# Kernel optimization log

Hardware: AMD Instinct MI355X
Metric: run time of the kernel (lower is better)

## Reference

```python
import jax, jax.numpy as jnp
import numpy as np

# Module hyperparameters (from init_kwargs)
N_HEAD = 16
D_K = 64
D_V = 64
TEMPERATURE = 0.7
TOP_K = 32
NEG_MIN = jnp.finfo(jnp.float32).min


def setup_inputs() -> dict:
    key = jax.random.key(0)
    ks = jax.random.split(key, 7)
    B, L, E = 2, 2048, 1024
    return {
        "q": jax.random.normal(ks[0], (B, L, E), jnp.float32),
        "k": jax.random.normal(ks[1], (B, L, E), jnp.float32),
        "v": jax.random.normal(ks[2], (B, L, D_V), jnp.float32),
        "w_q": jax.random.normal(ks[3], (N_HEAD * D_K, E), jnp.float32) * (E ** -0.5),
        "w_k": jax.random.normal(ks[4], (N_HEAD * D_K, E), jnp.float32) * (E ** -0.5),
        "w_v": jax.random.normal(ks[5], (N_HEAD * D_V, D_V), jnp.float32) * (D_V ** -0.5),
        "w_fc": jax.random.normal(ks[6], (D_V, N_HEAD * D_V), jnp.float32) * ((N_HEAD * D_V) ** -0.5),
    }


def _topk_restrict(logits):
    # Keep exactly TOP_K entries per row (scatter of top-k indices), fill rest with dtype min.
    B, H, Lq, Lk = logits.shape
    _, idx = jax.lax.top_k(logits, TOP_K)  # [B,H,Lq,TOP_K]
    bb = jnp.arange(B)[:, None, None, None]
    hh = jnp.arange(H)[None, :, None, None]
    qq = jnp.arange(Lq)[None, None, :, None]
    keep = jnp.zeros(logits.shape, bool).at[bb, hh, qq, idx].set(True)
    return jnp.where(keep, logits, NEG_MIN)


def reference(q, k, v, w_q, w_k, w_v, w_fc):
    B, Lq, _ = q.shape
    Lk = k.shape[1]
    Lv = v.shape[1]
    # Projections (bias-free linears), split heads: [B, H, L, d]
    q_proj = (q @ w_q.T).reshape(B, Lq, N_HEAD, D_K).transpose(0, 2, 1, 3)
    k_proj = (k @ w_k.T).reshape(B, Lk, N_HEAD, D_K).transpose(0, 2, 1, 3)
    v_proj = (v @ w_v.T).reshape(B, Lv, N_HEAD, D_V).transpose(0, 2, 1, 3)
    # Scaled QK^T in float32, then temperature scaling.
    logits = jnp.einsum("bhqd,bhkd->bhqk", q_proj / (D_K ** 0.5), k_proj).astype(jnp.float32)
    logits = logits / TEMPERATURE
    # Top-k restriction of attention logits (query_mask_flat=None -> applied to all queries).
    logits = _topk_restrict(logits)
    # Softmax selection; dropout is identity in eval / p=0.
    attn_probs = jax.nn.softmax(logits, axis=-1).astype(v.dtype)
    mixed = jnp.einsum("bhqk,bhkd->bhqd", attn_probs, v_proj)
    out = mixed.transpose(0, 2, 1, 3).reshape(B, Lq, N_HEAD * D_V)
    output = out @ w_fc.T
    return output, attn_probs
```

## Files before the change

### kernel.cpp

```cpp
#include <hip/hip_runtime.h>
#include <stdint.h>
#include <float.h>

constexpr int L = 2048;
constexpr int H = 16;
constexpr float SCALE = 0.17857142857142858f;
constexpr int OUT0 = 2 * 2048 * 64;
constexpr float QSTEP = 0.0625f;

typedef float f32x4 __attribute__((ext_vector_type(4)));
typedef short s16x8 __attribute__((ext_vector_type(8)));
typedef unsigned short u16x8 __attribute__((ext_vector_type(8)));
typedef _Float16 h16x8 __attribute__((ext_vector_type(8)));

__device__ __forceinline__ unsigned f2sort(float f) {
  unsigned u = __float_as_uint(f);
  return (u & 0x80000000u) ? ~u : (u | 0x80000000u);
}
__device__ __forceinline__ void lds_fence() {
  __asm__ __volatile__("s_waitcnt lgkmcnt(0)" ::: "memory");
}

__device__ __forceinline__ int wave_isum_dpp(int x) {
#define DPP_ADDI(CTRL) x += __builtin_amdgcn_update_dpp(0, x, CTRL, 0xf, 0xf, true);
  DPP_ADDI(0x111) DPP_ADDI(0x112) DPP_ADDI(0x114)
  DPP_ADDI(0x118) DPP_ADDI(0x142) DPP_ADDI(0x143)
#undef DPP_ADDI
  return __builtin_amdgcn_readlane(x, 63);
}
__device__ __forceinline__ float wave_fsum_dpp(float x) {
  int xi = __builtin_bit_cast(int, x);
#define DPP_ADDF(CTRL)                                                      \
  {                                                                         \
    int _s = __builtin_amdgcn_update_dpp(0, xi, CTRL, 0xf, 0xf, true);      \
    x = x + __builtin_bit_cast(float, _s);                                  \
    xi = __builtin_bit_cast(int, x);                                        \
  }
  DPP_ADDF(0x111) DPP_ADDF(0x112) DPP_ADDF(0x114)
  DPP_ADDF(0x118) DPP_ADDF(0x142) DPP_ADDF(0x143)
#undef DPP_ADDF
  return __builtin_bit_cast(float, __builtin_amdgcn_readlane(xi, 63));
}
__device__ __forceinline__ float wave_fmax_dpp(float x) {
  int xi = __builtin_bit_cast(int, x);
#define DPP_MAXF(CTRL)                                                      \
  {                                                                         \
    int _s = __builtin_amdgcn_update_dpp(xi, xi, CTRL, 0xf, 0xf, false);    \
    x = fmaxf(x, __builtin_bit_cast(float, _s));                            \
    xi = __builtin_bit_cast(int, x);                                        \
  }
  DPP_MAXF(0x111) DPP_MAXF(0x112) DPP_MAXF(0x114)
  DPP_MAXF(0x118) DPP_MAXF(0x142) DPP_MAXF(0x143)
#undef DPP_MAXF
  return __builtin_bit_cast(float, __builtin_amdgcn_readlane(xi, 63));
}
__device__ __forceinline__ int wave_imin_dpp(int x) {
#define DPP_MINI(CTRL)                                                      \
  {                                                                         \
    int _s = __builtin_amdgcn_update_dpp(x, x, CTRL, 0xf, 0xf, false);      \
    x = min(x, _s);                                                         \
  }
  DPP_MINI(0x111) DPP_MINI(0x112) DPP_MINI(0x114)
  DPP_MINI(0x118) DPP_MINI(0x142) DPP_MINI(0x143)
#undef DPP_MINI
  return __builtin_amdgcn_readlane(x, 63);
}

__device__ __forceinline__ void gload_lds16(const void* g, void* l) {
  __builtin_amdgcn_global_load_lds((const __attribute__((address_space(1))) void*)g,
                                   (__attribute__((address_space(3))) void*)l, 16, 0, 0);
}

__global__ __launch_bounds__(256) void split_kernel(
    const float* __restrict__ q, const float* __restrict__ k,
    const float* __restrict__ wq, const float* __restrict__ wk,
    unsigned short* __restrict__ qh, unsigned short* __restrict__ ql,
    unsigned short* __restrict__ kh, unsigned short* __restrict__ kl,
    unsigned short* __restrict__ wqh, unsigned short* __restrict__ wql,
    unsigned short* __restrict__ wkh, unsigned short* __restrict__ wkl) {
  const int y = blockIdx.y;
  const float* src = (y == 0) ? q : (y == 1) ? k : (y == 2) ? wq : wk;
  unsigned short* dh = (y == 0) ? qh : (y == 1) ? kh : (y == 2) ? wqh : wkh;
  unsigned short* dl = (y == 0) ? ql : (y == 1) ? kl : (y == 2) ? wql : wkl;
  const int n = (y < 2) ? (4096 * 1024) : (1024 * 1024);
  int idx = (blockIdx.x * 256 + threadIdx.x) * 4;
  const int stride = gridDim.x * 256 * 4;
  for (; idx < n; idx += stride) {
    float4 v = *(const float4*)(src + idx);
    float xs[4] = {v.x, v.y, v.z, v.w};
    unsigned short hs[4], ls[4];
#pragma unroll
    for (int i = 0; i < 4; ++i) {
      float x = xs[i] * 256.0f;
      _Float16 hh = (_Float16)x;
      float r = x - (float)hh;
      _Float16 ll = (_Float16)r;
      hs[i] = __builtin_bit_cast(unsigned short, hh);
      ls[i] = __builtin_bit_cast(unsigned short, ll);
    }
    *(ushort4*)(dh + idx) = make_ushort4(hs[0], hs[1], hs[2], hs[3]);
    *(ushort4*)(dl + idx) = make_ushort4(ls[0], ls[1], ls[2], ls[3]);
  }
}

__global__ __launch_bounds__(256, 2) void proj_split_kernel(
    const unsigned short* __restrict__ QH, const unsigned short* __restrict__ QL,
    const unsigned short* __restrict__ KH, const unsigned short* __restrict__ KL,
    const unsigned short* __restrict__ WQH, const unsigned short* __restrict__ WQL,
    const unsigned short* __restrict__ WKH, const unsigned short* __restrict__ WKL,
    float* __restrict__ QP, float* __restrict__ KP,
    unsigned short* __restrict__ Q16, unsigned short* __restrict__ K16) {
  __shared__ unsigned short sh[4][128 * 64];
  const int t = threadIdx.x;
  const int z = blockIdx.z;
  const int m0 = blockIdx.y * 128;
  const int n0 = blockIdx.x * 128;
  const unsigned short* xh = z ? KH : QH;
  const unsigned short* xl = z ? KL : QL;
  const unsigned short* wh = z ? WKH : WQH;
  const unsigned short* wl = z ? WKL : WQL;
  float* Y = z ? KP : QP;
  unsigned short* Y16 = z ? K16 : Q16;
  const unsigned short* mats[4] = {xh + (size_t)m0 * 1024, xl + (size_t)m0 * 1024,
                                   wh + (size_t)n0 * 1024, wl + (size_t)n0 * 1024};
  const int wv = t >> 6, lane = t & 63;
  const int wm = (wv & 1) * 64, wn = (wv >> 1) * 64;
  const int fr = lane & 15, quad = lane >> 4;
  f32x4 acc[16];
#pragma unroll
  for (int i = 0; i < 16; ++i) acc[i] = (f32x4){0.f, 0.f, 0.f, 0.f};

#define STAGE(cc)                                                              \
  {                                                                            \
    const int k0s = (cc) * 64;                                                 \
    _Pragma("unroll") for (int j = 0; j < 16; ++j) {                           \
      const int mat = j >> 2;                                                  \
      const int idx = (j & 3) * 256 + t;                                       \
      const int r = idx >> 3, p = idx & 7;                                     \
      const int sb = p ^ (r & 7);                                              \
      gload_lds16(mats[mat] + (size_t)r * 1024 + k0s + sb * 8, &sh[mat][idx * 8]); \
    }                                                                          \
  }

  STAGE(0);
  for (int c = 0; c < 16; ++c) {
    __syncthreads();
    h16x8 ah[2][4], alv[2][4], bh[2][4], blv[2][4];
#pragma unroll
    for (int kh2 = 0; kh2 < 2; ++kh2) {
#pragma unroll
      for (int mi = 0; mi < 4; ++mi) {
        int row = wm + mi * 16 + fr;
        int pp = (kh2 * 4 + quad) ^ (row & 7);
        ah[kh2][mi]  = *(const h16x8*)&sh[0][row * 64 + pp * 8];
        alv[kh2][mi] = *(const h16x8*)&sh[1][row * 64 + pp * 8];
      }
#pragma unroll
      for (int ni = 0; ni < 4; ++ni) {
        int row = wn + ni * 16 + fr;
        int pp = (kh2 * 4 + quad) ^ (row & 7);
        bh[kh2][ni]  = *(const h16x8*)&sh[2][row * 64 + pp * 8];
        blv[kh2][ni] = *(const h16x8*)&sh[3][row * 64 + pp * 8];
      }
    }
    __syncthreads();
    if (c < 15) STAGE(c + 1);
#pragma unroll
    for (int kh2 = 0; kh2 < 2; ++kh2)
#pragma unroll
      for (int mi = 0; mi < 4; ++mi)
#pragma unroll
        for (int ni = 0; ni < 4; ++ni) {
          acc[mi * 4 + ni] = __builtin_amdgcn_mfma_f32_16x16x32_f16(ah[kh2][mi], bh[kh2][ni], acc[mi * 4 + ni], 0, 0, 0);
          acc[mi * 4 + ni] = __builtin_amdgcn_mfma_f32_16x16x32_f16(ah[kh2][mi], blv[kh2][ni], acc[mi * 4 + ni], 0, 0, 0);
          acc[mi * 4 + ni] = __builtin_amdgcn_mfma_f32_16x16x32_f16(alv[kh2][mi], bh[kh2][ni], acc[mi * 4 + ni], 0, 0, 0);
        }
  }
#undef STAGE
#pragma unroll
  for (int mi = 0; mi < 4; ++mi)
#pragma unroll
    for (int ni = 0; ni < 4; ++ni) {
      int col = n0 + wn + ni * 16 + fr;
      int h = col >> 6, d = col & 63;
#pragma unroll
      for (int r = 0; r < 4; ++r) {
        int m = m0 + wm + mi * 16 + quad * 4 + r;
        int b = m >> 11, l = m & 2047;
        size_t off = (((size_t)b * H + h) * L + l) * 64 + d;
        float val = acc[mi * 4 + ni][r] * (1.0f / 65536.0f);
        Y[off] = val;
        _Float16 hf = (_Float16)val;
        Y16[off] = __builtin_bit_cast(unsigned short, hf);
      }
    }
}

template <int K, bool EMIT>
__global__ __launch_bounds__(256) void proj_kernel(const float* __restrict__ X,
                                                   const float* __restrict__ W,
                                                   float* __restrict__ Y,
                                                   unsigned short* __restrict__ Yb,
                                                   float bscale) {
  __shared__ float As[16][128];
  __shared__ float Bs[16][64];
  const int t = threadIdx.x;
  const int tx = t & 15;
  const int ty = t >> 4;
  const int m0 = blockIdx.y * 128;
  const int n0 = blockIdx.x * 64;
  const int ar = t >> 1, ac = (t & 1) * 8;
  const int br = t >> 2, bc = (t & 3) * 4;
  const float* xg = X + (size_t)(m0 + ar) * K + ac;
  const float* wg = W + (size_t)(n0 + br) * K + bc;
  float acc[8][4] = {};
  for (int k0 = 0; k0 < K; k0 += 16) {
    float4 a0 = *(const float4*)(xg + k0);
    float4 a1 = *(const float4*)(xg + k0 + 4);
    float4 b0 = *(const float4*)(wg + k0);
    __syncthreads();
    As[ac + 0][ar] = a0.x; As[ac + 1][ar] = a0.y; As[ac + 2][ar] = a0.z; As[ac + 3][ar] = a0.w;
    As[ac + 4][ar] = a1.x; As[ac + 5][ar] = a1.y; As[ac + 6][ar] = a1.z; As[ac + 7][ar] = a1.w;
    Bs[bc + 0][br] = b0.x; Bs[bc + 1][br] = b0.y; Bs[bc + 2][br] = b0.z; Bs[bc + 3][br] = b0.w;
    __syncthreads();
#pragma unroll
    for (int kk = 0; kk < 16; ++kk) {
      float4 av0 = *(const float4*)&As[kk][ty * 8];
      float4 av1 = *(const float4*)&As[kk][ty * 8 + 4];
      float4 bv = *(const float4*)&Bs[kk][tx * 4];
      float ar8[8] = {av0.x, av0.y, av0.z, av0.w, av1.x, av1.y, av1.z, av1.w};
      float br4[4] = {bv.x, bv.y, bv.z, bv.w};
#pragma unroll
      for (int i = 0; i < 8; ++i)
#pragma unroll
        for (int j = 0; j < 4; ++j) acc[i][j] = fmaf(ar8[i], br4[j], acc[i][j]);
    }
  }
  const int n = n0 + tx * 4;
  const int h = n >> 6, d = n & 63;
#pragma unroll
  for (int i = 0; i < 8; ++i) {
    int mm = m0 + ty * 8 + i;
    int b = mm >> 11, l = mm & 2047;
    size_t off = (((size_t)b * H + h) * L + l) * 64 + d;
    *(float4*)&Y[off] = make_float4(acc[i][0], acc[i][1], acc[i][2], acc[i][3]);
  }
}

constexpr int ALD = 72;
constexpr int CTB = 136;

__global__ __launch_bounds__(256) void alogits_kernel(const unsigned short* __restrict__ Qb,
                                                      const unsigned short* __restrict__ Kb,
                                                      char* __restrict__ AL) {
  __shared__ union {
    unsigned short qk[2][128 * ALD];
    char ct[128 * CTB];
  } sh;
  const int t = threadIdx.x;
  const int bh = blockIdx.z;
  const int m0 = blockIdx.y * 128, n0 = blockIdx.x * 128;
  const unsigned short* Qg = Qb + (size_t)bh * L * 64 + (size_t)m0 * 64;
  const unsigned short* Kg = Kb + (size_t)bh * L * 64 + (size_t)n0 * 64;
#pragma unroll
  for (int i = 0; i < 4; ++i) {
    int blk = t * 4 + i;
    int r = blk >> 3, lb = blk & 7;
    *(u16x8*)&sh.qk[0][r * ALD + lb * 8] = *(const u16x8*)&Qg[r * 64 + lb * 8];
    *(u16x8*)&sh.qk[1][r * ALD + lb * 8] = *(const u16x8*)&Kg[r * 64 + lb * 8];
  }
  __syncthreads();
  const int wv = t >> 6, lane = t & 63;
  const int wm = (wv & 1) * 64, wn = (wv >> 1) * 64;
  const int fr = lane & 15, quad = lane >> 4;
  f32x4 acc[16];
#pragma unroll
  for (int i = 0; i < 16; ++i) acc[i] = (f32x4){0.f, 0.f, 0.f, 0.f};
#pragma unroll
  for (int kh = 0; kh < 2; ++kh) {
    h16x8 a[4], b[4];
#pragma unroll
    for (int mi = 0; mi < 4; ++mi)
      a[mi] = *(const h16x8*)&sh.qk[0][(wm + mi * 16 + fr) * ALD + kh * 32 + quad * 8];
#pragma unroll
    for (int ni = 0; ni < 4; ++ni)
      b[ni] = *(const h16x8*)&sh.qk[1][(wn + ni * 16 + fr) * ALD + kh * 32 + quad * 8];
#pragma unroll
    for (int mi = 0; mi < 4; ++mi)
#pragma unroll
      for (int ni = 0; ni < 4; ++ni)
        acc[mi * 4 + ni] = __builtin_amdgcn_mfma_f32_16x16x32_f16(
            a[mi], b[ni], acc[mi * 4 + ni], 0, 0, 0);
  }
  __syncthreads();
#pragma unroll
  for (int mi = 0; mi < 4; ++mi)
#pragma unroll
    for (int ni = 0; ni < 4; ++ni) {
      int col = wn + ni * 16 + fr;
#pragma unroll
      for (int r = 0; r < 4; ++r) {
        int rowl = wm + mi * 16 + quad * 4 + r;
        float sc = acc[mi * 4 + ni][r] * 2.8571428571428572f;
        sc = fminf(fmaxf(sc, -127.0f), 127.0f);
        sh.ct[rowl * CTB + col] = (char)__float2int_rn(sc);
      }
    }
  __syncthreads();
  char* Abase = AL + (size_t)bh * L * L;
  const int rq = lane >> 4;
  const int cq = (lane & 15) * 8;
#pragma unroll
  for (int it = 0; it < 8; ++it) {
    int row = wv * 32 + it * 4 + rq;
    uint2 v8 = *(const uint2*)&sh.ct[row * CTB + cq];
    __builtin_nontemporal_store(v8.x, (unsigned*)&Abase[(size_t)(m0 + row) * L + n0 + cq]);
    __builtin_nontemporal_store(v8.y, (unsigned*)&Abase[(size_t)(m0 + row) * L + n0 + cq + 4]);
  }
}

__global__ __launch_bounds__(256) void select_kernel(const char* __restrict__ AL,
                                                     const float* __restrict__ Qp,
                                                     const float* __restrict__ Kp,
                                                     const float* __restrict__ Vp,
                                                     float* __restrict__ Probs,
                                                     float* __restrict__ Mixed) {
  __shared__ float prow[4][2048];
  __shared__ float qbuf[4][64];
  __shared__ int ibufc[4][64];
  __shared__ float pbuf[4][32];
  __shared__ int ibuf[4][32];
  const int lane = threadIdx.x & 63;
  const int w = threadIdx.x >> 6;
  const int row = blockIdx.x * 4 + w;
  const int bh = row >> 11;
  const int q = row & 2047;
  const unsigned long long below = (lane == 63) ? 0x7fffffffffffffffull
                                                : ((1ull << lane) - 1ull);
  const unsigned* Arow = (const unsigned*)(AL + (size_t)row * 2048);

  int li[32];
#pragma unroll
  for (int u2 = 0; u2 < 8; ++u2) {
    unsigned dw = __builtin_nontemporal_load(Arow + u2 * 64 + lane);
#pragma unroll
    for (int b = 0; b < 4; ++b)
      li[u2 * 4 + b] = (int)((char)(dw >> (8 * b)));
  }
#pragma unroll
  for (int u = 0; u < 32; ++u) prow[w][u * 64 + lane] = 0.f;
  if (lane < 16)
    *(float4*)&qbuf[w][lane * 4] = *(const float4*)&Qp[((size_t)bh * L + q) * 64 + lane * 4];

  int tlo = -128, thi = 128;
#pragma unroll
  for (int it = 0; it < 8; ++it) {
    int mid = (tlo + thi) >> 1;
    int c = 0;
#pragma unroll
    for (int u = 0; u < 32; ++u) c += (li[u] >= mid) ? 1 : 0;
    c = wave_isum_dpp(c);
    if (c >= 32) tlo = mid; else thi = mid;
  }
  const int t32 = tlo;

  int theta = t32;
  int c2 = 0;
  const int margs[5] = {6, 4, 2, 1, 0};
#pragma unroll
  for (int a = 0; a < 5; ++a) {
    int th = t32 - margs[a];
    int c = 0;
#pragma unroll
    for (int u = 0; u < 32; ++u) c += (li[u] >= th) ? 1 : 0;
    c = wave_isum_dpp(c);
    theta = th; c2 = c;
    if (c <= 64) break;
  }
  if (c2 > 64) c2 = 64;

  {
    int base = 0;
#pragma unroll
    for (int u = 0; u < 32; ++u) {
      bool cd = li[u] >= theta;
      unsigned long long mk = __ballot(cd);
      if (cd) {
        int s = base + __popcll(mk & below);
        if (s < 64) ibufc[w][s] = ((u >> 2) * 64 + lane) * 4 + (u & 3);
      }
      base += __popcll(mk);
    }
  }
  lds_fence();

  int myi = (lane < c2) ? ibufc[w][lane] : 0x7fffffff;
  float vex = -FLT_MAX;
  if (lane < c2) {
    const float4* K4 = (const float4*)(Kp + ((size_t)bh * L + myi) * 64);
    const float4* Q4 = (const float4*)&qbuf[w][0];
    float acc = 0.f;
#pragma unroll
    for (int dq = 0; dq < 16; ++dq) {
      float4 kv = K4[dq];
      float4 qv = Q4[dq];
      acc = fmaf(qv.x, kv.x, acc);
      acc = fmaf(qv.y, kv.y, acc);
      acc = fmaf(qv.z, kv.z, acc);
      acc = fmaf(qv.w, kv.w, acc);
    }
    vex = (acc * 0.125f) / 0.7f;
  }

  const unsigned sk = f2sort(vex);
  unsigned tb = 0;
#pragma unroll
  for (int bit = 31; bit >= 0; --bit) {
    unsigned cand = tb | (1u << bit);
    int cnt = (int)__popcll(__ballot(sk >= cand));
    if (cnt >= 32) tb = cand;
  }
  bool kept = sk > tb;
  {
    int cnt_gt = (int)__popcll(__ballot(kept));
    int need = 32 - cnt_gt;
    unsigned long long tiem = __ballot(sk == tb);
    if ((int)__popcll(tiem) <= need) {
      kept = kept || (sk == tb);
    } else {
      bool isT = (sk == tb);
      for (int r = 0; r < need; ++r) {
        int mi = wave_imin_dpp(isT ? myi : 0x7fffffff);
        if (isT && myi == mi) { kept = true; isT = false; }
      }
    }
  }

  float vmax = wave_fmax_dpp(vex);
  float e = kept ? __expf(vex - vmax) : 0.f;
  float S = wave_fsum_dpp(e);
  float p = e / S;
  {
    unsigned long long km = __ballot(kept);
    int slot = (int)__popcll(km & below);
    if (kept) {
      pbuf[w][slot] = p;
      ibuf[w][slot] = myi;
      prow[w][myi] = p;
    }
  }
  lds_fence();

  float* Prow = Probs + (size_t)row * 2048;
#pragma unroll
  for (int u = 0; u < 32; ++u)
    __builtin_nontemporal_store(prow[w][u * 64 + lane], Prow + u * 64 + lane);

  const float* Vb = Vp + (size_t)bh * L * 64;
  float accv = 0.f;
#pragma unroll
  for (int i = 0; i < 32; ++i)
    accv = fmaf(pbuf[w][i], Vb[(size_t)ibuf[w][i] * 64 + lane], accv);
  const int bb = bh >> 4, hh = bh & 15;
  Mixed[((size_t)(bb * 2048 + q)) * 1024 + hh * 64 + lane] = accv;
}

__global__ __launch_bounds__(256) void fc_kernel(const float* __restrict__ Mx,
                                                 const float* __restrict__ Wfc,
                                                 float* __restrict__ Out) {
  __shared__ float As[32][64];
  __shared__ float Ws[64][64];
  const int t = threadIdx.x;
  const int tx = t & 15;
  const int ty = t >> 4;
  const int m0 = blockIdx.x * 32;
  float acc[2][4] = {};
  for (int k0 = 0; k0 < 1024; k0 += 64) {
    __syncthreads();
    {
      int lin = t * 8;
      int rr = lin >> 6, kk = lin & 63;
      *(float4*)&As[rr][kk] = *(const float4*)&Mx[(size_t)(m0 + rr) * 1024 + k0 + kk];
      *(float4*)&As[rr][kk + 4] = *(const float4*)&Mx[(size_t)(m0 + rr) * 1024 + k0 + kk + 4];
    }
    {
      int n = t >> 2;
      int kq = (t & 3) * 16;
#pragma unroll
      for (int u = 0; u < 4; ++u) {
        float4 wv = *(const float4*)&Wfc[(size_t)n * 1024 + k0 + kq + u * 4];
        Ws[kq + u * 4 + 0][n] = wv.x;
        Ws[kq + u * 4 + 1][n] = wv.y;
        Ws[kq + u * 4 + 2][n] = wv.z;
        Ws[kq + u * 4 + 3][n] = wv.w;
      }
    }
    __syncthreads();
#pragma unroll
    for (int kk = 0; kk < 64; ++kk) {
      float a0 = As[ty][kk], a1 = As[ty + 16][kk];
      float4 wv = *(const float4*)&Ws[kk][tx * 4];
      float wr[4] = {wv.x, wv.y, wv.z, wv.w};
#pragma unroll
      for (int j = 0; j < 4; ++j) {
        acc[0][j] = fmaf(a0, wr[j], acc[0][j]);
        acc[1][j] = fmaf(a1, wr[j], acc[1][j]);
      }
    }
  }
#pragma unroll
  for (int i = 0; i < 2; ++i) {
    int mm = m0 + ty + i * 16;
    *(float4*)&Out[(size_t)mm * 64 + tx * 4] =
        make_float4(acc[i][0], acc[i][1], acc[i][2], acc[i][3]);
  }
}

extern "C" void kernel_launch(void* const* d_in, const int* in_sizes, int n_in,
                              void* d_out, int out_size, void* d_ws, size_t ws_size,
                              hipStream_t stream) {
  const float* q    = (const float*)d_in[0];
  const float* k    = (const float*)d_in[1];
  const float* v    = (const float*)d_in[2];
  const float* w_q  = (const float*)d_in[3];
  const float* w_k  = (const float*)d_in[4];
  const float* w_v  = (const float*)d_in[5];
  const float* w_fc = (const float*)d_in[6];

  float* out = (float*)d_out;
  float* probs = out + OUT0;

  float* ws = (float*)d_ws;
  float* q_proj = ws;
  float* k_proj = ws + 4194304;
  float* v_proj = ws + 8388608;
  float* mixed  = ws + 12582912;
  unsigned short* qb = (unsigned short*)(ws + 16777216);
  unsigned short* kb = (unsigned short*)(ws + 18874368);
  char* al = (char*)(ws + 20971520);

  unsigned short* qh  = (unsigned short*)((char*)d_ws + 234881024);
  unsigned short* ql  = qh + 4194304;
  unsigned short* kh  = ql + 4194304;
  unsigned short* kl  = kh + 4194304;
  unsigned short* wqh = kl + 4194304;
  unsigned short* wql = wqh + 1048576;
  unsigned short* wkh = wql + 1048576;
  unsigned short* wkl = wkh + 1048576;

  dim3 blk(256);
  split_kernel<<<dim3(1024, 4), blk, 0, stream>>>(q, k, w_q, w_k,
                                                  qh, ql, kh, kl, wqh, wql, wkh, wkl);
  proj_split_kernel<<<dim3(8, 32, 2), blk, 0, stream>>>(qh, ql, kh, kl,
                                                        wqh, wql, wkh, wkl,
                                                        q_proj, k_proj, qb, kb);
  proj_kernel<64, false><<<dim3(16, 32), blk, 0, stream>>>(v, w_v, v_proj, nullptr, 1.0f);
  alogits_kernel<<<dim3(16, 16, 32), blk, 0, stream>>>(qb, kb, al);
  select_kernel<<<dim3(16384), blk, 0, stream>>>(al, q_proj, k_proj, v_proj, probs, mixed);
  fc_kernel<<<dim3(128), blk, 0, stream>>>(mixed, w_fc, out);
}
```

Measured before the change: 855.2 us.

## Split select kernel into top-k selection and scatter/PV kernels

The select kernel no longer holds a 32KB shared-memory probability row or writes the dense probs and PV product. It now emits 32 (index, prob) pairs per row to a workspace buffer, and a new scatter_pv_kernel builds the dense row, writes probs and computes the V mix. The int8 logit stores and loads also switch from nontemporal to regular accesses, which may let the logits stay in cache between kernels. The split frees LDS so the selection stage can run at higher occupancy, at the cost of an extra launch and a pair round-trip through memory.

```diff
diff --git a/kernel.cpp b/kernel.cpp
--- a/kernel.cpp
+++ b/kernel.cpp
@@ -314,22 +314,17 @@
   for (int it = 0; it < 8; ++it) {
     int row = wv * 32 + it * 4 + rq;
     uint2 v8 = *(const uint2*)&sh.ct[row * CTB + cq];
-    __builtin_nontemporal_store(v8.x, (unsigned*)&Abase[(size_t)(m0 + row) * L + n0 + cq]);
-    __builtin_nontemporal_store(v8.y, (unsigned*)&Abase[(size_t)(m0 + row) * L + n0 + cq + 4]);
+    *(unsigned*)&Abase[(size_t)(m0 + row) * L + n0 + cq] = v8.x;
+    *(unsigned*)&Abase[(size_t)(m0 + row) * L + n0 + cq + 4] = v8.y;
   }
 }
 
 __global__ __launch_bounds__(256) void select_kernel(const char* __restrict__ AL,
                                                      const float* __restrict__ Qp,
                                                      const float* __restrict__ Kp,
-                                                     const float* __restrict__ Vp,
-                                                     float* __restrict__ Probs,
-                                                     float* __restrict__ Mixed) {
-  __shared__ float prow[4][2048];
+                                                     uint2* __restrict__ Pairs) {
   __shared__ float qbuf[4][64];
   __shared__ int ibufc[4][64];
-  __shared__ float pbuf[4][32];
-  __shared__ int ibuf[4][32];
   const int lane = threadIdx.x & 63;
   const int w = threadIdx.x >> 6;
   const int row = blockIdx.x * 4 + w;
@@ -342,13 +337,11 @@
   int li[32];
 #pragma unroll
   for (int u2 = 0; u2 < 8; ++u2) {
-    unsigned dw = __builtin_nontemporal_load(Arow + u2 * 64 + lane);
+    unsigned dw = Arow[u2 * 64 + lane];
 #pragma unroll
     for (int b = 0; b < 4; ++b)
       li[u2 * 4 + b] = (int)((char)(dw >> (8 * b)));
   }
-#pragma unroll
-  for (int u = 0; u < 32; ++u) prow[w][u * 64 + lane] = 0.f;
   if (lane < 16)
     *(float4*)&qbuf[w][lane * 4] = *(const float4*)&Qp[((size_t)bh * L + q) * 64 + lane * 4];
 
@@ -443,11 +436,33 @@
   {
     unsigned long long km = __ballot(kept);
     int slot = (int)__popcll(km & below);
-    if (kept) {
-      pbuf[w][slot] = p;
-      ibuf[w][slot] = myi;
-      prow[w][myi] = p;
-    }
+    if (kept)
+      Pairs[(size_t)row * 32 + slot] = make_uint2((unsigned)myi, __float_as_uint(p));
+  }
+}
+
+__global__ __launch_bounds__(256) void scatter_pv_kernel(const uint2* __restrict__ Pairs,
+                                                         const float* __restrict__ Vp,
+                                                         float* __restrict__ Probs,
+                                                         float* __restrict__ Mixed) {
+  __shared__ float prow[4][2048];
+  __shared__ float pbuf[4][32];
+  __shared__ int ibuf[4][32];
+  const int lane = threadIdx.x & 63;
+  const int w = threadIdx.x >> 6;
+  const int row = blockIdx.x * 4 + w;
+  const int bh = row >> 11;
+  const int q = row & 2047;
+
+#pragma unroll
+  for (int u = 0; u < 32; ++u) prow[w][u * 64 + lane] = 0.f;
+  if (lane < 32) {
+    uint2 pr = Pairs[(size_t)row * 32 + lane];
+    int idx = (int)pr.x;
+    float p = __uint_as_float(pr.y);
+    ibuf[w][lane] = idx;
+    pbuf[w][lane] = p;
+    prow[w][idx] = p;
   }
   lds_fence();
 
@@ -547,6 +562,7 @@
   unsigned short* wql = wqh + 1048576;
   unsigned short* wkh = wql + 1048576;
   unsigned short* wkl = wkh + 1048576;
+  uint2* pairs = (uint2*)((char*)d_ws + 276824064);
 
   dim3 blk(256);
   split_kernel<<<dim3(1024, 4), blk, 0, stream>>>(q, k, w_q, w_k,
@@ -556,6 +572,7 @@
                                                         q_proj, k_proj, qb, kb);
   proj_kernel<64, false><<<dim3(16, 32), blk, 0, stream>>>(v, w_v, v_proj, nullptr, 1.0f);
   alogits_kernel<<<dim3(16, 16, 32), blk, 0, stream>>>(qb, kb, al);
-  select_kernel<<<dim3(16384), blk, 0, stream>>>(al, q_proj, k_proj, v_proj, probs, mixed);
+  select_kernel<<<dim3(16384), blk, 0, stream>>>(al, q_proj, k_proj, pairs);
+  scatter_pv_kernel<<<dim3(16384), blk, 0, stream>>>(pairs, v_proj, probs, mixed);
   fc_kernel<<<dim3(128), blk, 0, stream>>>(mixed, w_fc, out);
 }
```

Measured after the change: 853.9 us. No clear change (-0.2%).
